# Optimization experiments

Hardware: AMD Instinct MI355X
Metric: run time of the kernel (lower is better)

## Reference

```python
import jax, jax.numpy as jnp
import numpy as np

DIM = 512
NUM_HEADS = 16
WIN = (7, 7)
N = WIN[0] * WIN[1]          # 49 tokens per window
NW = 64                      # windows per image
B = 32                       # images
B_ = B * NW                  # total windows = 2048
SCALE = (DIM // NUM_HEADS) ** -0.5


def _relative_position_index(wh, ww):
    coords = np.stack(np.meshgrid(np.arange(wh), np.arange(ww), indexing='ij'))  # (2, wh, ww)
    coords = coords.reshape(2, -1)                                               # (2, N)
    rel = coords[:, :, None] - coords[:, None, :]                                # (2, N, N)
    rel = rel.transpose(1, 2, 0).astype(np.int32)                                # (N, N, 2)
    rel[:, :, 0] += wh - 1
    rel[:, :, 1] += ww - 1
    rel[:, :, 0] *= 2 * ww - 1
    return jnp.asarray(rel.sum(-1), dtype=jnp.int32)                             # (N, N)


def _shift_mask(nw, n):
    # Swin-style additive mask: 0 within groups, -100 across groups.
    rng = np.random.RandomState(0)
    groups = rng.randint(0, 4, size=(nw, n)).astype(np.int32)
    m = np.where(groups[:, :, None] == groups[:, None, :], 0.0, -100.0)
    return jnp.asarray(m, dtype=jnp.float32)                                     # (nW, N, N)


def setup_inputs() -> dict:
    key = jax.random.key(0)
    ks = jax.random.split(key, 5)
    x = jax.random.normal(ks[0], (B_, N, DIM), dtype=jnp.float32)
    qkv_w = jax.random.normal(ks[1], (3 * DIM, DIM), dtype=jnp.float32) * 0.02
    qkv_b = jnp.zeros((3 * DIM,), dtype=jnp.float32)
    proj_w = jax.random.normal(ks[2], (DIM, DIM), dtype=jnp.float32) * 0.02
    proj_b = jnp.zeros((DIM,), dtype=jnp.float32)
    rpb_table = jax.random.normal(ks[3], ((2 * WIN[0] - 1) * (2 * WIN[1] - 1), NUM_HEADS), dtype=jnp.float32) * 0.02
    mask = _shift_mask(NW, N)
    rel_idx = _relative_position_index(*WIN)
    return {"x": x, "mask": mask, "qkv_w": qkv_w, "qkv_b": qkv_b,
            "proj_w": proj_w, "proj_b": proj_b, "rpb_table": rpb_table,
            "rel_idx": rel_idx}


def reference(x, mask, qkv_w, qkv_b, proj_w, proj_b, rpb_table, rel_idx):
    b_, n, c = x.shape
    nh = rpb_table.shape[1]
    d = c // nh
    # qkv projection: (B_, N, 3, nH, d) -> q, k, v each (B_, nH, N, d)
    qkv = (jnp.einsum('bnc,oc->bno', x, qkv_w) + qkv_b).reshape(b_, n, 3, nh, d)
    qkv = jnp.transpose(qkv, (2, 0, 3, 1, 4))
    q, k, v = qkv[0], qkv[1], qkv[2]
    attn = jnp.einsum('bhnd,bhmd->bhnm', q * SCALE, k)                     # (B_, nH, N, N)
    # gathered relative position bias: (N*N, nH) -> (nH, N, N)
    bias = rpb_table[rel_idx.reshape(-1)].reshape(n, n, nh)
    attn = attn + jnp.transpose(bias, (2, 0, 1))[None]
    # shifted-window mask add
    nw = mask.shape[0]
    attn = attn.reshape(b_ // nw, nw, nh, n, n) + mask[None, :, None]
    attn = attn.reshape(b_, nh, n, n)
    attn = jax.nn.softmax(attn, axis=-1)
    out = jnp.einsum('bhnm,bhmd->bhnd', attn, v)                           # (B_, nH, N, d)
    out = jnp.transpose(out, (0, 2, 1, 3)).reshape(b_, n, c)
    return jnp.einsum('bnc,oc->bno', out, proj_w) + proj_b
```

## Files before the change

kernel.cpp:

```cpp
#include <hip/hip_runtime.h>
#include <hip/hip_bf16.h>
#include <stdint.h>
#include <stddef.h>

#define B_TOT   2048
#define NTOK    49
#define CDIM    512
#define NHEAD   16
#define HD      32
#define NWIN    64
#define MROWS   (B_TOT*NTOK)
#define O_QKV   1536
#define SCALE_F 0.17677669529663687f

typedef short bf16x8 __attribute__((ext_vector_type(8)));
typedef float f32x4  __attribute__((ext_vector_type(4)));

__device__ __forceinline__ unsigned short f2bf(float f){
  union { float f; unsigned u; } v; v.f = f;
  unsigned r = v.u + 0x7fffu + ((v.u >> 16) & 1u);
  return (unsigned short)(r >> 16);
}
__device__ __forceinline__ unsigned pkbf(float a, float b){
  return (unsigned)f2bf(a) | ((unsigned)f2bf(b) << 16);
}

#define GL16(g,l) __builtin_amdgcn_global_load_lds( \
      (const __attribute__((address_space(1))) unsigned int*)(g), \
      (__attribute__((address_space(3))) unsigned int*)(l), 16, 0, 0)

__global__ void k_prep(const float* __restrict__ x,
                       const float* __restrict__ qkv_w, const float* __restrict__ proj_w,
                       const float* __restrict__ rpb, const int* __restrict__ rel_idx,
                       const float* __restrict__ mask,
                       unsigned short* __restrict__ xb,
                       unsigned short* __restrict__ wqkv, unsigned short* __restrict__ wproj,
                       float* __restrict__ bmb){
  int i = blockIdx.x * blockDim.x + threadIdx.x;
  int st = gridDim.x * blockDim.x;
  const int n4 = MROWS * CDIM / 4;
  for (int j = i; j < n4; j += st){
    float4 v = ((const float4*)x)[j];
    uint2 o;
    o.x = pkbf(v.x, v.y);
    o.y = pkbf(v.z, v.w);
    ((uint2*)xb)[j] = o;
  }
  for (int j = i; j < O_QKV*CDIM; j += st) wqkv[j] = f2bf(qkv_w[j]);
  for (int j = i; j < CDIM*CDIM;  j += st) wproj[j] = f2bf(proj_w[j]);
  const int TOT = NWIN * NHEAD * NTOK * 64;
  for (int j = i; j < TOT; j += st){
    int wh  = j / (NTOK*64);
    int rem = j - wh * (NTOK*64);
    int qt  = rem >> 6, kt = rem & 63;
    int wi = wh >> 4, h = wh & 15;
    float v;
    if (kt < NTOK){
      int rc = qt * NTOK + kt;
      v = mask[wi * (NTOK*NTOK) + rc] + rpb[rel_idx[rc] * NHEAD + h];
    } else v = -1e30f;
    bmb[j] = v;
  }
}

#define LDA_(P,RG,MI,S) (*(const bf16x8*)(rA + (P)*32768 + (RG)*16384 + (MI)*2048 + ((S)?(cb0^64):cb0)))
#define LDB_(P,CG,NI,S) (*(const bf16x8*)(rB + (P)*32768 + (CG)*16384 + (NI)*2048 + ((S)?(cb0^64):cb0)))

#define STAGE_A(P,HG,KT) { \
    GL16(aS0 + (size_t)(HG)*64*Kb + (size_t)(KT)*128, ldA + (P)*32768 + (HG)*16384); \
    GL16(aS1 + (size_t)(HG)*64*Kb + (size_t)(KT)*128, ldA + (P)*32768 + (HG)*16384 + 8192); }
#define STAGE_B(P,HG,KT) { \
    GL16(bS0 + (size_t)(HG)*32*Kb + (size_t)(KT)*128, ldB + (P)*32768 + (HG)*16384); \
    GL16(bS1 + (size_t)(HG)*32*Kb + (size_t)(KT)*128, ldB + (P)*32768 + (HG)*16384 + 8192); }

#define PHASE(P,RG,CG,DOA,DOB,VM,...) { \
  if (DOA){ _Pragma("unroll") for (int mi=0;mi<4;++mi){ af[mi][0]=LDA_(P,RG,mi,0); af[mi][1]=LDA_(P,RG,mi,1);} } \
  if (DOB){ _Pragma("unroll") for (int ni=0;ni<2;++ni){ bf_[ni][0]=LDB_(P,CG,ni,0); bf_[ni][1]=LDB_(P,CG,ni,1);} } \
  __VA_ARGS__; \
  __builtin_amdgcn_s_barrier(); \
  asm volatile("s_waitcnt lgkmcnt(0)" ::: "memory"); \
  __builtin_amdgcn_sched_barrier(0); \
  __builtin_amdgcn_s_setprio(1); \
  _Pragma("unroll") for (int s=0;s<2;++s) \
    _Pragma("unroll") for (int mi=0;mi<4;++mi) \
      _Pragma("unroll") for (int ni=0;ni<2;++ni) \
        acc[(RG)*4+mi][(CG)*2+ni] = __builtin_amdgcn_mfma_f32_16x16x32_bf16(af[mi][s], bf_[ni][s], acc[(RG)*4+mi][(CG)*2+ni], 0,0,0); \
  __builtin_amdgcn_s_setprio(0); \
  if (VM) asm volatile("s_waitcnt vmcnt(4)" ::: "memory"); \
  __builtin_amdgcn_s_barrier(); \
  asm volatile("" ::: "memory"); \
}

template<int OUT_F32>
__global__ __launch_bounds__(512, 2) void k_gemm8(const unsigned short* __restrict__ Ag,
                                                  const unsigned short* __restrict__ Bg,
                                                  const float* __restrict__ bias,
                                                  void* __restrict__ Cout,
                                                  int Ndim, int Kdim){
  extern __shared__ char smem[];
  const int tid = threadIdx.x;
  const int wv = tid >> 6, lane = tid & 63, lg = lane >> 4, lr = lane & 15;
  const int wm = wv >> 2, wn = wv & 3;

  const int nbx = gridDim.x;
  const int nwg = nbx * gridDim.y;
  const int id  = blockIdx.y * nbx + blockIdx.x;
  const int nid = (id & 7) * (nwg >> 3) + (id >> 3);
  const int bx = nid % nbx, by = nid / nbx;
  const int bm0 = by * 256, bn0 = bx * 256;
  const size_t Kb = (size_t)Kdim * 2;
  const int NIT = Kdim >> 7;

  const int srow = tid >> 3;
  const int scb  = ((tid & 7) << 4) ^ ((srow & 7) << 4);
  const char* aS0 = (const char*)Ag + (size_t)(bm0 + srow) * Kb + scb;
  const char* aS1 = (const char*)Ag + (size_t)(bm0 + 128 + srow) * Kb + scb;
  const char* bS0 = (const char*)Bg + (size_t)(bn0 + (srow>>5)*64 + (srow&31)) * Kb + scb;
  const char* bS1 = (const char*)Bg + (size_t)(bn0 + 128 + (srow>>5)*64 + (srow&31)) * Kb + scb;
  char* ldA = smem + wv * 1024;
  char* ldB = smem + 65536 + wv * 1024;

  const int cb0 = (lg * 16) ^ ((lr & 7) << 4);
  const char* rA = smem + (wm*64 + lr) * 128;
  const char* rB = smem + 65536 + (wn*32 + lr) * 128;

  f32x4 acc[8][4];
  #pragma unroll
  for (int i = 0; i < 8; ++i)
    #pragma unroll
    for (int j = 0; j < 4; ++j)
      #pragma unroll
      for (int r = 0; r < 4; ++r) acc[i][j][r] = 0.f;

  bf16x8 af[4][2], bf_[2][2];

  STAGE_A(0,0,0); STAGE_A(0,1,0); STAGE_B(0,0,0); STAGE_B(0,1,0);
  STAGE_A(1,0,1); STAGE_B(1,1,1);
  asm volatile("s_waitcnt vmcnt(4)" ::: "memory");
  __builtin_amdgcn_s_barrier();
  asm volatile("" ::: "memory");

  for (int it = 0; it < NIT; ++it){
    const int T = 2*it;
    PHASE(0, 0,0, 1,1, 0, STAGE_A(1,1,(T+1)))
    PHASE(0, 0,1, 0,1, 0, STAGE_B(1,0,(T+1)))
    PHASE(0, 1,1, 1,0, 0, STAGE_A(0,0,(T+2)))
    PHASE(0, 1,0, 0,1, 1, STAGE_B(0,1,(T+2)))
    PHASE(1, 0,0, 1,1, 0, STAGE_A(0,1,(T+2)))
    PHASE(1, 0,1, 0,1, 0, STAGE_B(0,0,(T+2)))
    PHASE(1, 1,1, 1,0, 0, STAGE_A(1,0,(T+3)))
    PHASE(1, 1,0, 0,1, 1, STAGE_B(1,1,(T+3)))
  }

  #pragma unroll
  for (int RG = 0; RG < 2; ++RG)
    #pragma unroll
    for (int mi = 0; mi < 4; ++mi)
      #pragma unroll
      for (int CG = 0; CG < 2; ++CG)
        #pragma unroll
        for (int ni = 0; ni < 2; ++ni){
          f32x4 v = acc[RG*4+mi][CG*2+ni];
          const int col = bn0 + wn*64 + CG*32 + ni*16 + lr;
          const float bc = bias[col];
          #pragma unroll
          for (int r = 0; r < 4; ++r){
            const int row = bm0 + wm*128 + RG*64 + mi*16 + lg*4 + r;
            const float t = v[r] + bc;
            if (OUT_F32) ((float*)Cout)[(size_t)row * Ndim + col] = t;
            else ((unsigned short*)Cout)[(size_t)row * Ndim + col] = f2bf(t);
          }
        }
}

__global__ __launch_bounds__(256) void k_attn(const unsigned short* __restrict__ qkv,
                                              const float* __restrict__ bm,
                                              unsigned short* __restrict__ ao){
  __shared__ char lds[4][12288];
  const int wv = threadIdx.x >> 6, lane = threadIdx.x & 63;
  const int lg = lane >> 4, lr = lane & 15;
  const int gw = blockIdx.x * 4 + wv;
  const int w = gw >> 4, h = gw & 15, wi = w & (NWIN - 1);
  char* Vt = lds[wv];
  char* P  = lds[wv] + 4096;

  const unsigned short* base = qkv + (size_t)w * NTOK * O_QKV + h * HD;

  const int vkt = lane >> 2, vch = lane & 3;
  bf16x8 vld[4];
  #pragma unroll
  for (int t = 0; t < 4; ++t){
    int kt = 16*t + vkt; int kts = kt < NTOK ? kt : NTOK-1;
    vld[t] = *(const bf16x8*)(base + 1024 + (size_t)kts * O_QKV + vch * 8);
  }

  bf16x8 qf[4], kf[4];
  #pragma unroll
  for (int i = 0; i < 4; ++i){
    int t = 16*i + lr; int ts = t < NTOK ? t : NTOK-1;
    qf[i] = *(const bf16x8*)(base + (size_t)ts * O_QKV + lg*8);
    kf[i] = *(const bf16x8*)(base + 512 + (size_t)ts * O_QKV + lg*8);
  }

  const float* bmp = bm + (size_t)(wi * NHEAD + h) * (NTOK * 64);
  f32x4 bias[4][4];
  #pragma unroll
  for (int mi = 0; mi < 4; ++mi){
    int qt = 16*mi + lr; int qtc = qt < NTOK ? qt : NTOK-1;
    #pragma unroll
    for (int ni = 0; ni < 4; ++ni)
      bias[mi][ni] = *(const f32x4*)(bmp + qtc*64 + ni*16 + lg*4);
  }

  f32x4 z4 = {0.f, 0.f, 0.f, 0.f};
  f32x4 s2[4][4];
  #pragma unroll
  for (int ni = 0; ni < 4; ++ni)
    #pragma unroll
    for (int mi = 0; mi < 4; ++mi)
      s2[ni][mi] = __builtin_amdgcn_mfma_f32_16x16x32_bf16(kf[ni], qf[mi], z4, 0, 0, 0);

  #pragma unroll
  for (int t = 0; t < 4; ++t){
    int kt = 16*t + vkt;
    #pragma unroll
    for (int j = 0; j < 8; ++j){
      int d = vch*8 + j;
      int swz = ((d & 7) ^ (d >> 3)) & 7;
      int byte = d*128 + ((2*kt) ^ (swz << 4));
      *(unsigned short*)(Vt + byte) = (unsigned short)vld[t][j];
    }
  }

  #pragma unroll
  for (int mi = 0; mi < 4; ++mi){
    float v[4][4];
    float mx = -1e30f;
    #pragma unroll
    for (int ni = 0; ni < 4; ++ni)
      #pragma unroll
      for (int r = 0; r < 4; ++r){
        float t = s2[ni][mi][r] * SCALE_F + bias[mi][ni][r];
        v[ni][r] = t;
        mx = fmaxf(mx, t);
      }
    mx = fmaxf(mx, __shfl_xor(mx, 16));
    mx = fmaxf(mx, __shfl_xor(mx, 32));
    float sum = 0.f;
    #pragma unroll
    for (int ni = 0; ni < 4; ++ni)
      #pragma unroll
      for (int r = 0; r < 4; ++r){
        float p = __expf(v[ni][r] - mx);
        v[ni][r] = p;
        sum += p;
      }
    sum += __shfl_xor(sum, 16);
    sum += __shfl_xor(sum, 32);
    float rn = 1.0f / sum;
    const int qt = 16*mi + lr;
    #pragma unroll
    for (int ni = 0; ni < 4; ++ni){
      uint2 pw;
      pw.x = pkbf(v[ni][0]*rn, v[ni][1]*rn);
      pw.y = pkbf(v[ni][2]*rn, v[ni][3]*rn);
      int byte = qt*128 + ((32*ni + 8*lg) ^ ((lr & 7) << 4));
      *(uint2*)(P + byte) = pw;
    }
  }

  f32x4 o[4][2];
  #pragma unroll
  for (int mi = 0; mi < 4; ++mi)
    #pragma unroll
    for (int ni = 0; ni < 2; ++ni)
      #pragma unroll
      for (int r = 0; r < 4; ++r) o[mi][ni][r] = 0.f;

  #pragma unroll
  for (int s = 0; s < 2; ++s){
    bf16x8 pf[4], vf[2];
    #pragma unroll
    for (int mi = 0; mi < 4; ++mi)
      pf[mi] = *(const bf16x8*)(P + (16*mi + lr)*128 + ((64*s + 16*lg) ^ ((lr & 7) << 4)));
    #pragma unroll
    for (int ni = 0; ni < 2; ++ni){
      int d = 16*ni + lr;
      int swz = ((d & 7) ^ (d >> 3)) & 7;
      vf[ni] = *(const bf16x8*)(Vt + d*128 + ((64*s + 16*lg) ^ (swz << 4)));
    }
    #pragma unroll
    for (int mi = 0; mi < 4; ++mi)
      #pragma unroll
      for (int ni = 0; ni < 2; ++ni)
        o[mi][ni] = __builtin_amdgcn_mfma_f32_16x16x32_bf16(pf[mi], vf[ni], o[mi][ni], 0, 0, 0);
  }

  unsigned short* aop = ao + (size_t)w * NTOK * CDIM + h * HD;
  #pragma unroll
  for (int mi = 0; mi < 4; ++mi)
    #pragma unroll
    for (int ni = 0; ni < 2; ++ni)
      #pragma unroll
      for (int r = 0; r < 4; ++r){
        int row = 16*mi + 4*lg + r, col = 16*ni + lr;
        if (row < NTOK)
          aop[(size_t)row * CDIM + col] = f2bf(o[mi][ni][r]);
      }
}

extern "C" void kernel_launch(void* const* d_in, const int* in_sizes, int n_in,
                              void* d_out, int out_size, void* d_ws, size_t ws_size,
                              hipStream_t stream){
  const float* x      = (const float*)d_in[0];
  const float* mask   = (const float*)d_in[1];
  const float* qkv_w  = (const float*)d_in[2];
  const float* qkv_b  = (const float*)d_in[3];
  const float* proj_w = (const float*)d_in[4];
  const float* proj_b = (const float*)d_in[5];
  const float* rpb    = (const float*)d_in[6];
  const int*   rel_i  = (const int*)d_in[7];

  char* ws = (char*)d_ws;
  unsigned short* xb    = (unsigned short*)(ws);
  unsigned short* qkvb  = (unsigned short*)(ws + 102760448);
  unsigned short* wqkv  = (unsigned short*)(ws + 411041792);
  unsigned short* wproj = (unsigned short*)(ws + 412614656);
  float*          bmb   = (float*)(ws + 413138944);

  (void)hipFuncSetAttribute(reinterpret_cast<const void*>(&k_gemm8<0>),
                            hipFuncAttributeMaxDynamicSharedMemorySize, 131072);
  (void)hipFuncSetAttribute(reinterpret_cast<const void*>(&k_gemm8<1>),
                            hipFuncAttributeMaxDynamicSharedMemorySize, 131072);

  k_prep<<<2048, 256, 0, stream>>>(x, qkv_w, proj_w, rpb, rel_i, mask, xb, wqkv, wproj, bmb);
  k_gemm8<0><<<dim3(O_QKV/256, MROWS/256), 512, 131072, stream>>>(xb, wqkv, qkv_b, qkvb, O_QKV, CDIM);
  k_attn<<<(B_TOT * NHEAD) / 4, 256, 0, stream>>>(qkvb, bmb, xb);
  k_gemm8<1><<<dim3(CDIM/256, MROWS/256), 512, 131072, stream>>>(xb, wproj, proj_b, d_out, CDIM, CDIM);
}
```

Measured before the change: 491.9 us.

## Process two heads per wave in attention and prefetch second head's loads

Each wave in the attention kernel now handles two consecutive heads of a window instead of one, and the grid is halved to match. The second head's global loads for Q, K, V and bias are issued before the first head's PV product and store, so their latency overlaps with that compute. MFMA sections are also wrapped in s_setprio raises. In exchange there is more register pressure from the in-flight loads and fewer waves in flight overall.

```diff
diff --git a/kernel.cpp b/kernel.cpp
--- a/kernel.cpp
+++ b/kernel.cpp
@@ -173,140 +173,107 @@
         }
 }
 
+#define ATTN_LOADS(S, hh) \
+  const unsigned short* base##S = wb + (hh) * HD; \
+  bf16x8 vld##S[4], qf##S[4], kf##S[4]; \
+  _Pragma("unroll") for (int t = 0; t < 4; ++t){ \
+    int kt = 16*t + vkt; int kts = kt < NTOK ? kt : NTOK-1; \
+    vld##S[t] = *(const bf16x8*)(base##S + 1024 + (size_t)kts * O_QKV + vch * 8); } \
+  _Pragma("unroll") for (int i = 0; i < 4; ++i){ \
+    int t = 16*i + lr; int ts = t < NTOK ? t : NTOK-1; \
+    qf##S[i] = *(const bf16x8*)(base##S + (size_t)ts * O_QKV + lg*8); \
+    kf##S[i] = *(const bf16x8*)(base##S + 512 + (size_t)ts * O_QKV + lg*8); } \
+  const float* bmp##S = bm + (size_t)(wi * NHEAD + (hh)) * (NTOK * 64); \
+  f32x4 bias##S[4][4]; \
+  _Pragma("unroll") for (int mi = 0; mi < 4; ++mi){ \
+    int qt = 16*mi + lr; int qtc = qt < NTOK ? qt : NTOK-1; \
+    _Pragma("unroll") for (int ni = 0; ni < 4; ++ni) \
+      bias##S[mi][ni] = *(const f32x4*)(bmp##S + qtc*64 + ni*16 + lg*4); }
+
+#define ATTN_QKT(S) \
+  __builtin_amdgcn_s_setprio(1); \
+  _Pragma("unroll") for (int ni = 0; ni < 4; ++ni) \
+    _Pragma("unroll") for (int mi = 0; mi < 4; ++mi) \
+      s2[ni][mi] = __builtin_amdgcn_mfma_f32_16x16x32_bf16(kf##S[ni], qf##S[mi], z4, 0, 0, 0); \
+  __builtin_amdgcn_s_setprio(0);
+
+#define ATTN_VTWRITE(S) \
+  _Pragma("unroll") for (int t = 0; t < 4; ++t){ \
+    int kt = 16*t + vkt; \
+    _Pragma("unroll") for (int j = 0; j < 8; ++j){ \
+      int d = vch*8 + j; \
+      int swz = ((d & 7) ^ (d >> 3)) & 7; \
+      *(unsigned short*)(Vt + d*128 + ((2*kt) ^ (swz << 4))) = (unsigned short)vld##S[t][j]; } }
+
+#define ATTN_SOFTMAX(S) \
+  _Pragma("unroll") for (int mi = 0; mi < 4; ++mi){ \
+    float v[4][4]; float mx = -1e30f; \
+    _Pragma("unroll") for (int ni = 0; ni < 4; ++ni) \
+      _Pragma("unroll") for (int r = 0; r < 4; ++r){ \
+        float t = s2[ni][mi][r] * SCALE_F + bias##S[mi][ni][r]; \
+        v[ni][r] = t; mx = fmaxf(mx, t); } \
+    mx = fmaxf(mx, __shfl_xor(mx, 16)); \
+    mx = fmaxf(mx, __shfl_xor(mx, 32)); \
+    float sum = 0.f; \
+    _Pragma("unroll") for (int ni = 0; ni < 4; ++ni) \
+      _Pragma("unroll") for (int r = 0; r < 4; ++r){ \
+        float p = __expf(v[ni][r] - mx); v[ni][r] = p; sum += p; } \
+    sum += __shfl_xor(sum, 16); sum += __shfl_xor(sum, 32); \
+    float rn = 1.0f / sum; \
+    const int qt = 16*mi + lr; \
+    _Pragma("unroll") for (int ni = 0; ni < 4; ++ni){ \
+      uint2 pw; pw.x = pkbf(v[ni][0]*rn, v[ni][1]*rn); pw.y = pkbf(v[ni][2]*rn, v[ni][3]*rn); \
+      *(uint2*)(P + qt*128 + ((32*ni + 8*lg) ^ ((lr & 7) << 4))) = pw; } }
+
+#define ATTN_PV_STORE(hh) { \
+  f32x4 o[4][2]; \
+  _Pragma("unroll") for (int mi = 0; mi < 4; ++mi) \
+    _Pragma("unroll") for (int ni = 0; ni < 2; ++ni) \
+      _Pragma("unroll") for (int r = 0; r < 4; ++r) o[mi][ni][r] = 0.f; \
+  _Pragma("unroll") for (int s = 0; s < 2; ++s){ \
+    bf16x8 pf[4], vf[2]; \
+    _Pragma("unroll") for (int mi = 0; mi < 4; ++mi) \
+      pf[mi] = *(const bf16x8*)(P + (16*mi + lr)*128 + ((64*s + 16*lg) ^ ((lr & 7) << 4))); \
+    _Pragma("unroll") for (int ni = 0; ni < 2; ++ni){ \
+      int d = 16*ni + lr; int swz = ((d & 7) ^ (d >> 3)) & 7; \
+      vf[ni] = *(const bf16x8*)(Vt + d*128 + ((64*s + 16*lg) ^ (swz << 4))); } \
+    __builtin_amdgcn_s_setprio(1); \
+    _Pragma("unroll") for (int mi = 0; mi < 4; ++mi) \
+      _Pragma("unroll") for (int ni = 0; ni < 2; ++ni) \
+        o[mi][ni] = __builtin_amdgcn_mfma_f32_16x16x32_bf16(pf[mi], vf[ni], o[mi][ni], 0, 0, 0); \
+    __builtin_amdgcn_s_setprio(0); } \
+  unsigned short* aop = ao + (size_t)w * NTOK * CDIM + (hh) * HD; \
+  _Pragma("unroll") for (int mi = 0; mi < 4; ++mi) \
+    _Pragma("unroll") for (int ni = 0; ni < 2; ++ni) \
+      _Pragma("unroll") for (int r = 0; r < 4; ++r){ \
+        int row = 16*mi + 4*lg + r, col = 16*ni + lr; \
+        if (row < NTOK) aop[(size_t)row * CDIM + col] = f2bf(o[mi][ni][r]); } }
+
 __global__ __launch_bounds__(256) void k_attn(const unsigned short* __restrict__ qkv,
                                               const float* __restrict__ bm,
                                               unsigned short* __restrict__ ao){
   __shared__ char lds[4][12288];
   const int wv = threadIdx.x >> 6, lane = threadIdx.x & 63;
   const int lg = lane >> 4, lr = lane & 15;
-  const int gw = blockIdx.x * 4 + wv;
-  const int w = gw >> 4, h = gw & 15, wi = w & (NWIN - 1);
+  const int gw2 = blockIdx.x * 4 + wv;
+  const int w = gw2 >> 3, h0 = (gw2 & 7) << 1, wi = w & (NWIN - 1);
   char* Vt = lds[wv];
   char* P  = lds[wv] + 4096;
-
-  const unsigned short* base = qkv + (size_t)w * NTOK * O_QKV + h * HD;
-
+  const unsigned short* wb = qkv + (size_t)w * NTOK * O_QKV;
   const int vkt = lane >> 2, vch = lane & 3;
-  bf16x8 vld[4];
-  #pragma unroll
-  for (int t = 0; t < 4; ++t){
-    int kt = 16*t + vkt; int kts = kt < NTOK ? kt : NTOK-1;
-    vld[t] = *(const bf16x8*)(base + 1024 + (size_t)kts * O_QKV + vch * 8);
-  }
-
-  bf16x8 qf[4], kf[4];
-  #pragma unroll
-  for (int i = 0; i < 4; ++i){
-    int t = 16*i + lr; int ts = t < NTOK ? t : NTOK-1;
-    qf[i] = *(const bf16x8*)(base + (size_t)ts * O_QKV + lg*8);
-    kf[i] = *(const bf16x8*)(base + 512 + (size_t)ts * O_QKV + lg*8);
-  }
-
-  const float* bmp = bm + (size_t)(wi * NHEAD + h) * (NTOK * 64);
-  f32x4 bias[4][4];
-  #pragma unroll
-  for (int mi = 0; mi < 4; ++mi){
-    int qt = 16*mi + lr; int qtc = qt < NTOK ? qt : NTOK-1;
-    #pragma unroll
-    for (int ni = 0; ni < 4; ++ni)
-      bias[mi][ni] = *(const f32x4*)(bmp + qtc*64 + ni*16 + lg*4);
-  }
-
   f32x4 z4 = {0.f, 0.f, 0.f, 0.f};
   f32x4 s2[4][4];
-  #pragma unroll
-  for (int ni = 0; ni < 4; ++ni)
-    #pragma unroll
-    for (int mi = 0; mi < 4; ++mi)
-      s2[ni][mi] = __builtin_amdgcn_mfma_f32_16x16x32_bf16(kf[ni], qf[mi], z4, 0, 0, 0);
-
-  #pragma unroll
-  for (int t = 0; t < 4; ++t){
-    int kt = 16*t + vkt;
-    #pragma unroll
-    for (int j = 0; j < 8; ++j){
-      int d = vch*8 + j;
-      int swz = ((d & 7) ^ (d >> 3)) & 7;
-      int byte = d*128 + ((2*kt) ^ (swz << 4));
-      *(unsigned short*)(Vt + byte) = (unsigned short)vld[t][j];
-    }
-  }
-
-  #pragma unroll
-  for (int mi = 0; mi < 4; ++mi){
-    float v[4][4];
-    float mx = -1e30f;
-    #pragma unroll
-    for (int ni = 0; ni < 4; ++ni)
-      #pragma unroll
-      for (int r = 0; r < 4; ++r){
-        float t = s2[ni][mi][r] * SCALE_F + bias[mi][ni][r];
-        v[ni][r] = t;
-        mx = fmaxf(mx, t);
-      }
-    mx = fmaxf(mx, __shfl_xor(mx, 16));
-    mx = fmaxf(mx, __shfl_xor(mx, 32));
-    float sum = 0.f;
-    #pragma unroll
-    for (int ni = 0; ni < 4; ++ni)
-      #pragma unroll
-      for (int r = 0; r < 4; ++r){
-        float p = __expf(v[ni][r] - mx);
-        v[ni][r] = p;
-        sum += p;
-      }
-    sum += __shfl_xor(sum, 16);
-    sum += __shfl_xor(sum, 32);
-    float rn = 1.0f / sum;
-    const int qt = 16*mi + lr;
-    #pragma unroll
-    for (int ni = 0; ni < 4; ++ni){
-      uint2 pw;
-      pw.x = pkbf(v[ni][0]*rn, v[ni][1]*rn);
-      pw.y = pkbf(v[ni][2]*rn, v[ni][3]*rn);
-      int byte = qt*128 + ((32*ni + 8*lg) ^ ((lr & 7) << 4));
-      *(uint2*)(P + byte) = pw;
-    }
-  }
-
-  f32x4 o[4][2];
-  #pragma unroll
-  for (int mi = 0; mi < 4; ++mi)
-    #pragma unroll
-    for (int ni = 0; ni < 2; ++ni)
-      #pragma unroll
-      for (int r = 0; r < 4; ++r) o[mi][ni][r] = 0.f;
-
-  #pragma unroll
-  for (int s = 0; s < 2; ++s){
-    bf16x8 pf[4], vf[2];
-    #pragma unroll
-    for (int mi = 0; mi < 4; ++mi)
-      pf[mi] = *(const bf16x8*)(P + (16*mi + lr)*128 + ((64*s + 16*lg) ^ ((lr & 7) << 4)));
-    #pragma unroll
-    for (int ni = 0; ni < 2; ++ni){
-      int d = 16*ni + lr;
-      int swz = ((d & 7) ^ (d >> 3)) & 7;
-      vf[ni] = *(const bf16x8*)(Vt + d*128 + ((64*s + 16*lg) ^ (swz << 4)));
-    }
-    #pragma unroll
-    for (int mi = 0; mi < 4; ++mi)
-      #pragma unroll
-      for (int ni = 0; ni < 2; ++ni)
-        o[mi][ni] = __builtin_amdgcn_mfma_f32_16x16x32_bf16(pf[mi], vf[ni], o[mi][ni], 0, 0, 0);
-  }
-
-  unsigned short* aop = ao + (size_t)w * NTOK * CDIM + h * HD;
-  #pragma unroll
-  for (int mi = 0; mi < 4; ++mi)
-    #pragma unroll
-    for (int ni = 0; ni < 2; ++ni)
-      #pragma unroll
-      for (int r = 0; r < 4; ++r){
-        int row = 16*mi + 4*lg + r, col = 16*ni + lr;
-        if (row < NTOK)
-          aop[(size_t)row * CDIM + col] = f2bf(o[mi][ni][r]);
-      }
+
+  ATTN_LOADS(A, h0)
+  ATTN_QKT(A)
+  ATTN_VTWRITE(A)
+  ATTN_SOFTMAX(A)
+  ATTN_LOADS(B, h0 + 1)
+  ATTN_PV_STORE(h0)
+  ATTN_QKT(B)
+  ATTN_VTWRITE(B)
+  ATTN_SOFTMAX(B)
+  ATTN_PV_STORE(h0 + 1)
 }
 
 extern "C" void kernel_launch(void* const* d_in, const int* in_sizes, int n_in,
@@ -335,6 +302,6 @@
 
   k_prep<<<2048, 256, 0, stream>>>(x, qkv_w, proj_w, rpb, rel_i, mask, xb, wqkv, wproj, bmb);
   k_gemm8<0><<<dim3(O_QKV/256, MROWS/256), 512, 131072, stream>>>(xb, wqkv, qkv_b, qkvb, O_QKV, CDIM);
-  k_attn<<<(B_TOT * NHEAD) / 4, 256, 0, stream>>>(qkvb, bmb, xb);
+  k_attn<<<(B_TOT * NHEAD) / 8, 256, 0, stream>>>(qkvb, bmb, xb);
   k_gemm8<1><<<dim3(CDIM/256, MROWS/256), 512, 131072, stream>>>(xb, wproj, proj_b, d_out, CDIM, CDIM);
 }
```

Result: slower. 544.6 us (+10.7%).
